# Performance work log

Hardware: AMD Instinct MI355X
Metric: run time of the kernel (lower is better)

## Reference

```python
import jax, jax.numpy as jnp
import numpy as np

B, T, C, H = 128, 256, 512, 512

def setup_inputs() -> dict:
    key = jax.random.key(0)
    k1, k2, k3, k4 = jax.random.split(key, 4)
    x = jax.random.normal(k1, (B, T, C), dtype=jnp.float32)
    # nn.Linear(n_embed, H_size, bias=False).weight has shape [H, C]; scaled init
    s = 1.0 / np.sqrt(C)
    Wq = jax.random.normal(k2, (H, C), dtype=jnp.float32) * s
    Wk = jax.random.normal(k3, (H, C), dtype=jnp.float32) * s
    Wv = jax.random.normal(k4, (H, C), dtype=jnp.float32) * s
    return {"x": x, "Wq": Wq, "Wk": Wk, "Wv": Wv}

def reference(x, Wq, Wk, Wv):
    # q,k,v: [B,T,H] = x @ W.T (torch Linear convention)
    q = jnp.einsum('btc,hc->bth', x, Wq)
    k = jnp.einsum('btc,hc->bth', x, Wk)
    v = jnp.einsum('btc,hc->bth', x, Wv)
    scale = k.shape[-1] ** -0.5
    score = jnp.einsum('bqh,bkh->bqk', q, k) * scale  # [B,T,T]
    # causal mask: position j attends to i only if i <= j
    i = jnp.arange(T)
    causal = i[None, :] <= i[:, None]  # [T,T] lower-triangular
    score = jnp.where(causal[None, :, :], score, -jnp.inf)
    attn = jax.nn.softmax(score, axis=-1)
    # dropout is identity in eval mode
    out = jnp.einsum('bqk,bkh->bqh', attn, v)  # [B,T,H]
    return out
```

## Files before the change

### kernel.cpp

```cpp
#include <hip/hip_runtime.h>

#define B_ 128
#define T_ 256
#define C_ 512
#define H_ 512
#define CSCALE 0.063763824f

typedef _Float16 f16x8 __attribute__((ext_vector_type(8)));
typedef _Float16 f16x4 __attribute__((ext_vector_type(4)));
typedef _Float16 f16x2 __attribute__((ext_vector_type(2)));
typedef float    f32x4 __attribute__((ext_vector_type(4)));
typedef float    f32x16 __attribute__((ext_vector_type(16)));
typedef unsigned int u32;
typedef u32 u32x4 __attribute__((ext_vector_type(4)));

__device__ __forceinline__ void gld16(const void* gsrc, void* ldst) {
  __builtin_amdgcn_global_load_lds(
      (__attribute__((address_space(1))) void*)gsrc,
      (__attribute__((address_space(3))) void*)ldst, 16, 0, 0);
}

__global__ __launch_bounds__(256) void cvt_kernel(
    const float4* __restrict__ x, const float4* __restrict__ wq,
    const float4* __restrict__ wk, const float4* __restrict__ wv,
    f16x4* __restrict__ dst) {
  const int NX = (B_ * T_ * C_) / 4;
  const int NW = (H_ * C_) / 4;
  const int total = NX + 3 * NW;
  int gid = blockIdx.x * 256 + threadIdx.x;
  int gsz = gridDim.x * 256;
  for (int i = gid; i < total; i += gsz) {
    float4 f;
    if (i < NX)            f = x[i];
    else if (i < NX + NW)  f = wq[i - NX];
    else if (i < NX + 2*NW) f = wk[i - NX - NW];
    else                   f = wv[i - NX - 2*NW];
    f16x4 u = {(_Float16)f.x, (_Float16)f.y, (_Float16)f.z, (_Float16)f.w};
    dst[i] = u;
  }
}

__global__ __launch_bounds__(256) void proj_kernel(
    const _Float16* __restrict__ xh, const _Float16* __restrict__ wh,
    _Float16* __restrict__ qh, _Float16* __restrict__ kh,
    _Float16* __restrict__ vth) {
  __shared__ _Float16 As[128 * 32];
  __shared__ _Float16 Bs[128 * 32];

  const int tid  = threadIdx.x;
  const int lane = tid & 63;
  const int wave = tid >> 6;
  const int lr = lane & 15, lk = lane >> 4;
  const int m0 = blockIdx.x * 128;
  const int n0 = blockIdx.y * 128;
  const int z  = blockIdx.z;
  const _Float16* wz = wh + z * (H_ * C_);

  const int wm = (wave >> 1) * 64;
  const int wn = (wave & 1) * 64;

  f32x4 acc[4][4];
#pragma unroll
  for (int i = 0; i < 4; ++i)
#pragma unroll
    for (int j = 0; j < 4; ++j) acc[i][j] = {0.f, 0.f, 0.f, 0.f};

  const int srow = tid >> 2, scol = (tid & 3) * 8;
  const _Float16* aSrc = xh + (m0 + srow) * C_ + scol;
  const _Float16* bSrc = wz + (n0 + srow) * C_ + scol;

  for (int k0 = 0; k0 < C_; k0 += 32) {
    __syncthreads();
#pragma unroll
    for (int i = 0; i < 2; ++i) {
      gld16((const void*)(aSrc + i * 64 * C_ + k0), (void*)&As[i * 2048 + wave * 512]);
      gld16((const void*)(bSrc + i * 64 * C_ + k0), (void*)&Bs[i * 2048 + wave * 512]);
    }
    __syncthreads();

    f16x8 a[4], b[4];
#pragma unroll
    for (int mi = 0; mi < 4; ++mi)
      a[mi] = *(const f16x8*)&As[(wm + mi * 16 + lr) * 32 + lk * 8];
#pragma unroll
    for (int ni = 0; ni < 4; ++ni)
      b[ni] = *(const f16x8*)&Bs[(wn + ni * 16 + lr) * 32 + lk * 8];
#pragma unroll
    for (int mi = 0; mi < 4; ++mi)
#pragma unroll
      for (int ni = 0; ni < 4; ++ni)
        acc[mi][ni] = __builtin_amdgcn_mfma_f32_16x16x32_f16(a[mi], b[ni], acc[mi][ni], 0, 0, 0);
  }

  if (z < 2) {
    _Float16* out = (z == 0) ? qh : kh;
#pragma unroll
    for (int mi = 0; mi < 4; ++mi) {
      int mbase = m0 + wm + mi * 16 + lk * 4;
#pragma unroll
      for (int ni = 0; ni < 4; ++ni) {
        int n = n0 + wn + ni * 16 + lr;
#pragma unroll
        for (int r = 0; r < 4; ++r)
          out[(mbase + r) * H_ + n] = (_Float16)acc[mi][ni][r];
      }
    }
  } else {
#pragma unroll
    for (int mi = 0; mi < 4; ++mi) {
      int mbase = m0 + wm + mi * 16 + lk * 4;
      int bb = mbase >> 8, tt = mbase & 255;
#pragma unroll
      for (int ni = 0; ni < 4; ++ni) {
        int n = n0 + wn + ni * 16 + lr;
        f16x4 u = {(_Float16)acc[mi][ni][0], (_Float16)acc[mi][ni][1],
                   (_Float16)acc[mi][ni][2], (_Float16)acc[mi][ni][3]};
        *(f16x4*)&vth[bb * (H_ * T_) + n * T_ + tt] = u;
      }
    }
  }
}

__global__ __launch_bounds__(256, 2) void attn_kernel(
    const _Float16* __restrict__ qh, const _Float16* __restrict__ kh,
    const _Float16* __restrict__ vth, float* __restrict__ dout) {
  __shared__ f32x4 Ex[2][4][4][64];

  const int tid  = threadIdx.x;
  const int lane = tid & 63;
  const int wq   = tid >> 6;
  const int lq   = lane & 31;
  const int hi   = lane >> 5;
  const int flat = blockIdx.x;
  const int xcd  = flat & 7;
  const int rest = flat >> 3;
  const int qb   = 7 - (rest & 7);
  const int g    = rest >> 3;
  const int b    = xcd + (g << 3);
  const int q0   = qb * 32;
  const int nkv  = qb + 1;
  const int hbase = wq * 128;
  const int qg   = q0 + lq;

  f16x8 qf[8];
  const _Float16* qp = qh + ((size_t)b * T_ + qg) * H_ + hbase + hi * 8;
#pragma unroll
  for (int ks = 0; ks < 8; ++ks) qf[ks] = *(const f16x8*)&qp[ks * 16];

  f32x16 ot[4];
#pragma unroll
  for (int i = 0; i < 4; ++i) ot[i] = {};
  float m_ = -1e30f, l_ = 0.f;

  const _Float16* kp = kh  + ((size_t)b * T_ + lq) * H_ + hbase + hi * 8;
  const _Float16* vp = vth + ((size_t)b * H_ + hbase + lq) * T_ + hi * 8;

  for (int kvt = 0; kvt < nkv; ++kvt) {
    const int kv0 = kvt * 32;

    f16x8 kf[8];
#pragma unroll
    for (int ks = 0; ks < 8; ++ks)
      kf[ks] = *(const f16x8*)&kp[(size_t)kv0 * H_ + ks * 16];
    f32x16 st = {};
#pragma unroll
    for (int ks = 0; ks < 8; ++ks)
      st = __builtin_amdgcn_mfma_f32_32x32x16_f16(kf[ks], qf[ks], st, 0, 0, 0);

    const int buf = kvt & 1;
#pragma unroll
    for (int c = 0; c < 4; ++c) {
      f32x4 w4 = {st[c*4+0], st[c*4+1], st[c*4+2], st[c*4+3]};
      Ex[buf][wq][c][lane] = w4;
    }
    __syncthreads();
#pragma unroll
    for (int ow = 0; ow < 4; ++ow) {
      if (ow == wq) continue;
#pragma unroll
      for (int c = 0; c < 4; ++c) {
        f32x4 r4 = Ex[buf][ow][c][lane];
        st[c*4+0] += r4[0]; st[c*4+1] += r4[1];
        st[c*4+2] += r4[2]; st[c*4+3] += r4[3];
      }
    }

    float p[16], rm = -1e30f;
    const int kvb = kv0 + 4 * hi;
#pragma unroll
    for (int r = 0; r < 16; ++r) {
      int kvg = kvb + (r & 3) + 8 * (r >> 2);
      float v = (kvg > qg) ? -1e30f : st[r];
      p[r] = v;
      rm = fmaxf(rm, v);
    }
    rm = fmaxf(rm, __shfl_xor(rm, 32, 64));

    if (__any((int)(rm > m_ + 64.f))) {
      float mn = fmaxf(m_, rm);
      float al = __builtin_amdgcn_exp2f((m_ - mn) * CSCALE);
      m_ = mn; l_ *= al;
#pragma unroll
      for (int i = 0; i < 4; ++i)
#pragma unroll
        for (int e = 0; e < 16; ++e) ot[i][e] *= al;
    }
    float rs = 0.f;
#pragma unroll
    for (int r = 0; r < 16; ++r) {
      p[r] = __builtin_amdgcn_exp2f((p[r] - m_) * CSCALE);
      rs += p[r];
    }
    rs += __shfl_xor(rs, 32, 64);
    l_ += rs;

    u32 w[8], sw[8];
#pragma unroll
    for (int i = 0; i < 8; ++i) {
      f16x2 h2; h2[0] = (_Float16)p[2*i]; h2[1] = (_Float16)p[2*i+1];
      w[i] = __builtin_bit_cast(u32, h2);
    }
#pragma unroll
    for (int i = 0; i < 8; ++i) sw[i] = (u32)__shfl_xor((int)w[i], 32, 64);
    u32x4 t0 = { hi ? sw[2] : w[0],  hi ? sw[3] : w[1],
                 hi ? w[2]  : sw[0], hi ? w[3]  : sw[1] };
    u32x4 t1 = { hi ? sw[6] : w[4],  hi ? sw[7] : w[5],
                 hi ? w[6]  : sw[4], hi ? w[7]  : sw[5] };
    f16x8 pb0 = __builtin_bit_cast(f16x8, t0);
    f16x8 pb1 = __builtin_bit_cast(f16x8, t1);

#pragma unroll
    for (int ht = 0; ht < 4; ++ht) {
      f16x8 va0 = *(const f16x8*)&vp[(size_t)(ht * 32) * T_ + kv0];
      f16x8 va1 = *(const f16x8*)&vp[(size_t)(ht * 32) * T_ + kv0 + 16];
      ot[ht] = __builtin_amdgcn_mfma_f32_32x32x16_f16(va0, pb0, ot[ht], 0, 0, 0);
      ot[ht] = __builtin_amdgcn_mfma_f32_32x32x16_f16(va1, pb1, ot[ht], 0, 0, 0);
    }
  }

  float li = 1.0f / l_;
  float* op = dout + ((size_t)b * T_ + qg) * H_ + hbase + 4 * hi;
#pragma unroll
  for (int ht = 0; ht < 4; ++ht)
#pragma unroll
    for (int rq = 0; rq < 4; ++rq) {
      f32x4 v4 = {ot[ht][rq*4+0] * li, ot[ht][rq*4+1] * li,
                  ot[ht][rq*4+2] * li, ot[ht][rq*4+3] * li};
      *(f32x4*)&op[ht * 32 + rq * 8] = v4;
    }
}

extern "C" void kernel_launch(void* const* d_in, const int* in_sizes, int n_in,
                              void* d_out, int out_size, void* d_ws, size_t ws_size,
                              hipStream_t stream) {
  const size_t NXE = (size_t)B_ * T_ * C_;
  const size_t NWE = (size_t)3 * H_ * C_;
  const size_t NQE = (size_t)B_ * T_ * H_;
  const size_t need = (NXE + NWE + 3 * NQE) * sizeof(_Float16);
  if (ws_size < need) return;

  const float* x  = (const float*)d_in[0];
  const float* wq = (const float*)d_in[1];
  const float* wk = (const float*)d_in[2];
  const float* wv = (const float*)d_in[3];

  _Float16* xh  = (_Float16*)d_ws;
  _Float16* wh  = xh + NXE;
  _Float16* qh  = wh + NWE;
  _Float16* kh  = qh + NQE;
  _Float16* vth = kh + NQE;

  cvt_kernel<<<2048, 256, 0, stream>>>((const float4*)x, (const float4*)wq,
                                       (const float4*)wk, (const float4*)wv,
                                       (f16x4*)xh);
  proj_kernel<<<dim3(256, 4, 3), dim3(256), 0, stream>>>(xh, wh, qh, kh, vth);
  attn_kernel<<<1024, 256, 0, stream>>>(qh, kh, vth, (float*)d_out);
}
```

Baseline: 175.7 us.

## Rewrite projection GEMM with 256x256 tiles and double-buffered async LDS pipeline

The QKV projection kernel moves from 128x128 tiles with 4 waves and a single-stage sync-load-compute loop to 256x256 tiles with 8 waves. It uses a 128KB double-buffered LDS layout and an interleaved schedule where global-to-LDS loads for the next K chunk are issued between MFMA phases. Explicit vmcnt waits and s_setprio around the MFMA bursts are meant to overlap memory latency with compute and cut barrier stalls. The trade-off is a grid of 768 blocks and heavy LDS use, which limits occupancy and could cause load-balance issues across CUs.

```diff
diff --git a/kernel.cpp b/kernel.cpp
--- a/kernel.cpp
+++ b/kernel.cpp
@@ -40,82 +40,114 @@
   }
 }
 
-__global__ __launch_bounds__(256) void proj_kernel(
+__global__ __launch_bounds__(512, 2) void proj_kernel(
     const _Float16* __restrict__ xh, const _Float16* __restrict__ wh,
     _Float16* __restrict__ qh, _Float16* __restrict__ kh,
     _Float16* __restrict__ vth) {
-  __shared__ _Float16 As[128 * 32];
-  __shared__ _Float16 Bs[128 * 32];
+  __shared__ _Float16 L[65536];
 
   const int tid  = threadIdx.x;
   const int lane = tid & 63;
   const int wave = tid >> 6;
   const int lr = lane & 15, lk = lane >> 4;
-  const int m0 = blockIdx.x * 128;
-  const int n0 = blockIdx.y * 128;
+  const int lane8 = lane * 8;
+  const int wr = wave >> 2, wc = wave & 3;
+  const int m0 = blockIdx.x * 256;
+  const int n0 = blockIdx.y * 256;
   const int z  = blockIdx.z;
   const _Float16* wz = wh + z * (H_ * C_);
 
-  const int wm = (wave >> 1) * 64;
-  const int wn = (wave & 1) * 64;
-
-  f32x4 acc[4][4];
-#pragma unroll
-  for (int i = 0; i < 4; ++i)
+  const int srow = wave * 16 + lr;
+  const int scol = lk * 8;
+  const _Float16* aS = xh + (size_t)(m0 + srow) * C_ + scol;
+  const _Float16* bS = wz + (size_t)(n0 + srow) * C_ + scol;
+
+  f32x4 acc[8][4];
+#pragma unroll
+  for (int i = 0; i < 8; ++i)
 #pragma unroll
     for (int j = 0; j < 4; ++j) acc[i][j] = {0.f, 0.f, 0.f, 0.f};
-
-  const int srow = tid >> 2, scol = (tid & 3) * 8;
-  const _Float16* aSrc = xh + (m0 + srow) * C_ + scol;
-  const _Float16* bSrc = wz + (n0 + srow) * C_ + scol;
-
-  for (int k0 = 0; k0 < C_; k0 += 32) {
-    __syncthreads();
-#pragma unroll
-    for (int i = 0; i < 2; ++i) {
-      gld16((const void*)(aSrc + i * 64 * C_ + k0), (void*)&As[i * 2048 + wave * 512]);
-      gld16((const void*)(bSrc + i * 64 * C_ + k0), (void*)&Bs[i * 2048 + wave * 512]);
-    }
-    __syncthreads();
-
-    f16x8 a[4], b[4];
-#pragma unroll
-    for (int mi = 0; mi < 4; ++mi)
-      a[mi] = *(const f16x8*)&As[(wm + mi * 16 + lr) * 32 + lk * 8];
-#pragma unroll
-    for (int ni = 0; ni < 4; ++ni)
-      b[ni] = *(const f16x8*)&Bs[(wn + ni * 16 + lr) * 32 + lk * 8];
-#pragma unroll
-    for (int mi = 0; mi < 4; ++mi)
-#pragma unroll
-      for (int ni = 0; ni < 4; ++ni)
-        acc[mi][ni] = __builtin_amdgcn_mfma_f32_16x16x32_f16(a[mi], b[ni], acc[mi][ni], 0, 0, 0);
+  f16x8 af[4], bf[4];
+
+  gld16(aS,               &L[(wave) * 512]);
+  gld16(aS + 65536,       &L[(8 + wave) * 512]);
+  gld16(bS,               &L[16384 + (wave) * 512]);
+  gld16(bS + 65536,       &L[16384 + (8 + wave) * 512]);
+  gld16(aS + 32,          &L[(16 + wave) * 512]);
+  gld16(aS + 65536 + 32,  &L[(16 + 8 + wave) * 512]);
+  gld16(bS + 32,          &L[16384 + (16 + wave) * 512]);
+  gld16(bS + 65536 + 32,  &L[16384 + (16 + 8 + wave) * 512]);
+  asm volatile("s_waitcnt vmcnt(4)" ::: "memory");
+  __builtin_amdgcn_s_barrier();
+
+#define PH(BUF, MH, KH, STK, SKK, SBUF, SB, VM) do {                          \
+    if ((MH) == 0) {                                                           \
+      _Pragma("unroll") for (int ni = 0; ni < 4; ++ni)                         \
+        bf[ni] = *(const f16x8*)&L[(BUF) * 32768 + 16384 +                     \
+                                   ((KH) * 16 + wc * 4 + ni) * 512 + lane8];   \
+    }                                                                          \
+    _Pragma("unroll") for (int q = 0; q < 4; ++q)                              \
+      af[q] = *(const f16x8*)&L[(BUF) * 32768 +                                \
+                                ((KH) * 16 + wr * 8 + (MH) * 4 + q) * 512 +    \
+                                lane8];                                        \
+    {                                                                          \
+      const _Float16* s_ = (SB) ? bS : aS;                                     \
+      const int db_ = (SBUF) * 32768 + ((SB) ? 16384 : 0);                     \
+      gld16(s_ + (STK) + (SKK) * 32,                                           \
+            &L[db_ + ((SKK) * 16 + wave) * 512]);                              \
+      gld16(s_ + 65536 + (STK) + (SKK) * 32,                                   \
+            &L[db_ + ((SKK) * 16 + 8 + wave) * 512]);                          \
+    }                                                                          \
+    __builtin_amdgcn_s_barrier();                                              \
+    __builtin_amdgcn_s_setprio(1);                                             \
+    _Pragma("unroll") for (int q = 0; q < 4; ++q)                              \
+      _Pragma("unroll") for (int ni = 0; ni < 4; ++ni)                         \
+        acc[(MH) * 4 + q][ni] = __builtin_amdgcn_mfma_f32_16x16x32_f16(        \
+            af[q], bf[ni], acc[(MH) * 4 + q][ni], 0, 0, 0);                    \
+    __builtin_amdgcn_s_setprio(0);                                             \
+    if (VM) asm volatile("s_waitcnt vmcnt(4)" ::: "memory");                   \
+    __builtin_amdgcn_s_barrier();                                              \
+  } while (0)
+
+#pragma unroll 1
+  for (int it = 0; it < 4; ++it) {
+    const int k1 = (2 * it + 1) * 64;
+    const int k2 = (2 * it + 2 < 8 ? 2 * it + 2 : 7) * 64;
+    PH(0, 0, 0, k1, 0, 1, 0, 0);
+    PH(0, 1, 0, k1, 0, 1, 1, 1);
+    PH(0, 0, 1, k1, 1, 1, 0, 0);
+    PH(0, 1, 1, k1, 1, 1, 1, 1);
+    PH(1, 0, 0, k2, 0, 0, 0, 0);
+    PH(1, 1, 0, k2, 0, 0, 1, 1);
+    PH(1, 0, 1, k2, 1, 0, 0, 0);
+    PH(1, 1, 1, k2, 1, 0, 1, 1);
   }
+#undef PH
 
   if (z < 2) {
     _Float16* out = (z == 0) ? qh : kh;
 #pragma unroll
-    for (int mi = 0; mi < 4; ++mi) {
-      int mbase = m0 + wm + mi * 16 + lk * 4;
+    for (int mi = 0; mi < 8; ++mi) {
+      int mg = m0 + wr * 128 + mi * 16 + lk * 4;
 #pragma unroll
       for (int ni = 0; ni < 4; ++ni) {
-        int n = n0 + wn + ni * 16 + lr;
+        int n = n0 + wc * 64 + ni * 16 + lr;
 #pragma unroll
         for (int r = 0; r < 4; ++r)
-          out[(mbase + r) * H_ + n] = (_Float16)acc[mi][ni][r];
+          out[(size_t)(mg + r) * H_ + n] = (_Float16)acc[mi][ni][r];
       }
     }
   } else {
-#pragma unroll
-    for (int mi = 0; mi < 4; ++mi) {
-      int mbase = m0 + wm + mi * 16 + lk * 4;
-      int bb = mbase >> 8, tt = mbase & 255;
+    int bb = m0 >> 8;
+#pragma unroll
+    for (int mi = 0; mi < 8; ++mi) {
+      int ttb = wr * 128 + mi * 16 + lk * 4;
 #pragma unroll
       for (int ni = 0; ni < 4; ++ni) {
-        int n = n0 + wn + ni * 16 + lr;
+        int n = n0 + wc * 64 + ni * 16 + lr;
         f16x4 u = {(_Float16)acc[mi][ni][0], (_Float16)acc[mi][ni][1],
                    (_Float16)acc[mi][ni][2], (_Float16)acc[mi][ni][3]};
-        *(f16x4*)&vth[bb * (H_ * T_) + n * T_ + tt] = u;
+        *(f16x4*)&vth[(size_t)bb * (H_ * T_) + (size_t)n * T_ + ttb] = u;
       }
     }
   }
@@ -273,6 +305,6 @@
   cvt_kernel<<<2048, 256, 0, stream>>>((const float4*)x, (const float4*)wq,
                                        (const float4*)wk, (const float4*)wv,
                                        (f16x4*)xh);
-  proj_kernel<<<dim3(256, 4, 3), dim3(256), 0, stream>>>(xh, wh, qh, kh, vth);
+  proj_kernel<<<dim3(128, 2, 3), 512, 0, stream>>>(xh, wh, qh, kh, vth);
   attn_kernel<<<1024, 256, 0, stream>>>(qh, kh, vth, (float*)d_out);
 }
```

Result: faster. 171.9 us (-2.1%).
